# Optimization experiments

Measured on AMD Instinct MI355X. Metric: run time of the kernel, lower is better.

The kernel has to match this reference:

```python
import jax, jax.numpy as jnp
import numpy as np

NE, NR, D, H, L = 200000, 500, 128, 4, 2
HD = D // H
N, E, B = 32768, 262144, 256
MARGIN = 1.0


def setup_inputs() -> dict:
    key = jax.random.key(0)
    ks = jax.random.split(key, 16)
    nrm = lambda k, shp, s=0.05: jax.random.normal(k, shp, jnp.float32) * s
    inp = {
        'ent_emb': nrm(ks[0], (NE, D)),
        'rel_emb': nrm(ks[1], (NR, D)),
        'rel_prior': nrm(ks[2], (NR, 1)),
    }
    for i, nm in enumerate(['Wq', 'Wk', 'Wv', 'Wo', 'Wek', 'Wev']):
        inp[nm] = nrm(ks[3 + i], (L, D, D))
    for gi, g in enumerate(['h', 't', 'n']):
        kb = jax.random.fold_in(key, 100 + gi)
        k1, k2, k3, k4 = jax.random.split(kb, 4)
        inp[f'x_{g}'] = jax.random.randint(k1, (N,), 0, NE, jnp.int32)
        inp[f'ei_{g}'] = jax.random.randint(k2, (2, E), 0, N, jnp.int32)
        inp[f'ea_{g}'] = jax.random.randint(k3, (E,), 0, NR, jnp.int32)
        inp[f'y_{g}'] = jax.random.randint(k4, (B,), 0, N // B, jnp.int32)
        inp[f's_{g}'] = jnp.full((B,), N // B, dtype=jnp.int32)
    inp['sample'] = jax.random.randint(ks[9], (B, 3), 0, NR, jnp.int32)
    return inp


def gnn_embed(ent_emb, rel_emb, rel_prior, Wq, Wk, Wv, Wo, Wek, Wev, x, ei, ea, y, s):
    n = x.shape[0]
    h = ent_emb[x]                    # [N, D] node features (embedding lookup)
    e_emb = rel_emb[ea]               # [E, D] edge relation embedding
    e_pri = rel_prior[ea]             # [E, 1] scalar relation prior gate
    src, dst = ei[0], ei[1]
    scale = 1.0 / np.sqrt(HD).astype(np.float32)
    for l in range(L):
        q = (h @ Wq[l]).reshape(n, H, HD)[dst]                               # [E,H,HD]
        k = (h @ Wk[l]).reshape(n, H, HD)[src] + (e_emb @ Wek[l]).reshape(-1, H, HD)
        v = (h @ Wv[l]).reshape(n, H, HD)[src] + (e_emb @ Wev[l]).reshape(-1, H, HD)
        score = jnp.sum(q * k, axis=-1) * scale * e_pri                      # [E,H]
        # segment softmax over incoming edges of each destination node
        m = jax.ops.segment_max(score, dst, num_segments=n)
        m = jnp.where(jnp.isfinite(m), m, 0.0)
        ex = jnp.exp(score - m[dst])
        den = jax.ops.segment_sum(ex, dst, num_segments=n)[dst]
        alpha = ex / (den + 1e-16)                                           # [E,H]
        msg = jax.ops.segment_sum((alpha[..., None] * v).reshape(-1, D), dst, num_segments=n)
        h = jax.nn.gelu(h + msg @ Wo[l])                                     # residual + activation
    # get_real_index: exclusive cumsum of graph sizes + local target index
    offsets = jnp.concatenate([jnp.zeros((1,), s.dtype), jnp.cumsum(s)[:-1]])
    return h[offsets + y]             # [B, D]


def reference(ent_emb, rel_emb, rel_prior, Wq, Wk, Wv, Wo, Wek, Wev,
              x_h, ei_h, ea_h, y_h, s_h,
              x_t, ei_t, ea_t, y_t, s_t,
              x_n, ei_n, ea_n, y_n, s_n, sample):
    g = lambda x, ei, ea, y, s: gnn_embed(ent_emb, rel_emb, rel_prior, Wq, Wk, Wv, Wo, Wek, Wev, x, ei, ea, y, s)
    h = g(x_h, ei_h, ea_h, y_h, s_h)[:, None, :]   # [B,1,D]
    t = g(x_t, ei_t, ea_t, y_t, s_t)[:, None, :]
    tn = g(x_n, ei_n, ea_n, y_n, s_n)[:, None, :]
    r = rel_emb[sample[:, 1]][:, None, :]          # [B,1,D]
    proj_t = h + r                                 # TransE projection
    pos = jnp.linalg.norm(t - proj_t + 1e-8, axis=2)   # [B,1]
    negs = jnp.linalg.norm(t - tn + 1e-8, axis=2)      # [B,1]
    neg = jnp.mean(negs, axis=-1)                      # [B]
    # MarginRankingLoss(pos, neg, target=-1): mean(max(0, (pos-neg)+margin)); broadcasts [B,1]-[B] -> [B,B]
    loss = jnp.mean(jnp.maximum(pos - neg + MARGIN, 0.0))
    return loss
```

## Files before the change

### kernel.cpp

```cpp
#include <hip/hip_runtime.h>
#include <hip/hip_bf16.h>
#include <math.h>

#define NEC 200000
#define NRC 500
#define DD 128
#define LLC 2
#define NNODE 32768
#define EEDGE 262144
#define BBATCH 256
#define NG 3
#define BCAP 32

typedef __attribute__((ext_vector_type(8))) short short8;
typedef __attribute__((ext_vector_type(4))) float floatx4;
typedef __attribute__((ext_vector_type(4))) unsigned short ushort4v;

__device__ __forceinline__ float bf2f(unsigned short u) {
  union { unsigned int i; float f; } c; c.i = ((unsigned int)u) << 16; return c.f;
}
__device__ __forceinline__ unsigned short f2bf(float f) {
  union { float f; unsigned int i; } c; c.f = f;
  unsigned int x = c.i;
  unsigned int r = x + 0x7fffu + ((x >> 16) & 1u);
  return (unsigned short)(r >> 16);
}
__device__ __forceinline__ float bfu_lo(unsigned int u) {
  union { unsigned int i; float f; } c; c.i = u << 16; return c.f;
}
__device__ __forceinline__ float bfu_hi(unsigned int u) {
  union { unsigned int i; float f; } c; c.i = u & 0xffff0000u; return c.f;
}

__device__ __forceinline__ bool detect_fm(const void* ent) {
  unsigned int u = ((const unsigned int*)ent)[threadIdx.x & 63];
  bool big = fabsf(bfu_lo(u)) > 100.f;
  return __ballot(big) != 0ull;
}

__global__ __launch_bounds__(128) void k_prep(const void* ent, const void* rel,
    const void* prior, const void* Wq, const void* Wk, const void* Wv, const void* Wo,
    const void* Wek, const void* Wev,
    float* pris, unsigned short* WT, unsigned short* relk, unsigned short* relv) {
  bool fm = detect_fm(ent);
  int bid = blockIdx.x, tid = threadIdx.x;
  if (bid < 4) {
    int r = bid * 128 + tid;
    if (r < NRC) {
      float p = fm ? ((const float*)prior)[r] : bf2f(((const unsigned short*)prior)[r]);
      pris[r] = p * 0.17677669529663687f;
    }
  } else if (bid < 1028) {
    int t = (bid - 4) * 128 + tid;
    int mat = t >> 15;
    int rem = t & 32767;
    int l = rem >> 14;
    int p = rem & 16383;
    int d = p >> 7, c = p & 127;
    const void* W = mat == 0 ? Wq : (mat == 1 ? Wk : (mat == 2 ? Wv : Wo));
    size_t src = (size_t)l * DD * DD + (size_t)c * DD + d;
    float v = fm ? ((const float*)W)[src] : bf2f(((const unsigned short*)W)[src]);
    WT[(((size_t)mat * LLC + l) * DD + d) * DD + c] = f2bf(v);
  } else {
    int rid = bid - 1028;
    int which = rid / 1000;
    int l = (rid / 500) % 2;
    int r = rid % 500;
    int d = tid;
    size_t wofs = (size_t)l * DD * DD;
    const float* Wf = (const float*)(which ? Wev : Wek) + wofs;
    const unsigned short* Wb = (const unsigned short*)(which ? Wev : Wek) + wofs;
    __shared__ float re[DD];
    re[d] = fm ? ((const float*)rel)[r * DD + d] : bf2f(((const unsigned short*)rel)[r * DD + d]);
    __syncthreads();
    float acc = 0.f;
    if (fm) { for (int c = 0; c < DD; ++c) acc += re[c] * Wf[c * DD + d]; }
    else    { for (int c = 0; c < DD; ++c) acc += re[c] * bf2f(Wb[c * DD + d]); }
    unsigned short* out = which ? relv : relk;
    out[((size_t)l * NRC + r) * DD + d] = f2bf(acc);
  }
}

__global__ __launch_bounds__(256) void k_gb(const void* ent,
    const int* x0, const int* x1, const int* x2,
    const int* ei0, const int* ea0, const int* ei1, const int* ea1,
    const int* ei2, const int* ea2,
    unsigned short* hbf, int* deg, unsigned int* bucket) {
  int bid = blockIdx.x, tid = threadIdx.x;
  if (bid < 3072) {
    bool fm = detect_fm(ent);
    int rbase = bid * 32;
    int g = rbase >> 15;
    const int* x = g == 0 ? x0 : (g == 1 ? x1 : x2);
    int c = tid & 31;
    int j4 = tid >> 5;
    int rows[4], xs[4];
    #pragma unroll
    for (int k = 0; k < 4; ++k) {
      rows[k] = rbase + j4 + 8 * k;
      xs[k] = x[rows[k] & (NNODE - 1)];
    }
    if (fm) {
      float4 v[4];
      #pragma unroll
      for (int k = 0; k < 4; ++k)
        v[k] = *reinterpret_cast<const float4*>((const float*)ent + (size_t)xs[k] * DD + c * 4);
      #pragma unroll
      for (int k = 0; k < 4; ++k) {
        uint2 o;
        o.x = ((unsigned int)f2bf(v[k].y) << 16) | (unsigned int)f2bf(v[k].x);
        o.y = ((unsigned int)f2bf(v[k].w) << 16) | (unsigned int)f2bf(v[k].z);
        *reinterpret_cast<uint2*>(hbf + (size_t)rows[k] * DD + c * 4) = o;
      }
    } else {
      uint2 v[4];
      #pragma unroll
      for (int k = 0; k < 4; ++k)
        v[k] = *reinterpret_cast<const uint2*>((const unsigned short*)ent + (size_t)xs[k] * DD + c * 4);
      #pragma unroll
      for (int k = 0; k < 4; ++k)
        *reinterpret_cast<uint2*>(hbf + (size_t)rows[k] * DD + c * 4) = v[k];
    }
  } else {
    int bb = bid - 3072;
    int g = bb >> 10;
    const int* ei = g == 0 ? ei0 : (g == 1 ? ei1 : ei2);
    const int* ea = g == 0 ? ea0 : (g == 1 ? ea1 : ea2);
    int e = (bb & 1023) * 256 + tid;
    int dst = ei[EEDGE + e];
    int src = ei[e];
    int r = ea[e];
    int pos = atomicAdd(&deg[g * NNODE + dst], 1);
    if (pos < BCAP)
      bucket[((size_t)g * NNODE + dst) * BCAP + pos] = (unsigned int)src | ((unsigned int)r << 15);
  }
}

__device__ __forceinline__ void stage_wt(const unsigned short* WT, int tid,
                                         unsigned short (*Wt)[136]) {
  #pragma unroll
  for (int pass = 0; pass < 8; ++pass) {
    int idx = pass * 256 + tid;
    int d = idx >> 4, c0 = (idx & 15) << 3;
    *reinterpret_cast<short8*>(&Wt[d][c0]) =
        *reinterpret_cast<const short8*>(WT + d * DD + c0);
  }
}

__global__ __launch_bounds__(256) void k_gemm_qkv(const unsigned short* A,
    const unsigned short* WT, int layer, unsigned short* Qo, unsigned short* Ko,
    unsigned short* Vo) {
  __shared__ unsigned short Wt[DD][136];
  int mat = blockIdx.y;
  unsigned short* O = mat == 0 ? Qo : (mat == 1 ? Ko : Vo);
  int g = blockIdx.z;
  const unsigned short* Ag = A + (size_t)g * NNODE * DD;
  unsigned short* Og = O + (size_t)g * NNODE * DD;
  int tid = threadIdx.x;
  stage_wt(WT + ((size_t)mat * LLC + layer) * DD * DD, tid, Wt);
  __syncthreads();
  int w = tid >> 6, lane = tid & 63;
  int m = lane & 15, quad = lane >> 4;
  int row = blockIdx.x * 64 + w * 16 + m;
  floatx4 acc[8];
  #pragma unroll
  for (int t = 0; t < 8; ++t) acc[t] = (floatx4){0.f, 0.f, 0.f, 0.f};
  const unsigned short* arow = Ag + (size_t)row * DD;
  #pragma unroll
  for (int ks = 0; ks < 4; ++ks) {
    short8 a = *reinterpret_cast<const short8*>(arow + ks * 32 + quad * 8);
    #pragma unroll
    for (int t = 0; t < 8; ++t) {
      short8 b = *reinterpret_cast<const short8*>(&Wt[t * 16 + m][ks * 32 + quad * 8]);
      acc[t] = __builtin_amdgcn_mfma_f32_16x16x32_bf16(a, b, acc[t], 0, 0, 0);
    }
  }
  __syncthreads();
  unsigned short* ut = &Wt[0][0];
  #pragma unroll
  for (int t = 0; t < 8; ++t) {
    #pragma unroll
    for (int r = 0; r < 4; ++r) {
      ut[(w * 16 + quad * 4 + r) * 136 + t * 16 + m] = f2bf(acc[t][r]);
    }
  }
  __syncthreads();
  int rowbase = blockIdx.x * 64;
  #pragma unroll
  for (int k = 0; k < 4; ++k) {
    int flat = k * 256 + tid;
    int rw = flat >> 4, c8 = flat & 15;
    short8 v = *reinterpret_cast<const short8*>(ut + rw * 136 + c8 * 8);
    *reinterpret_cast<short8*>(Og + (size_t)(rowbase + rw) * DD + c8 * 8) = v;
  }
}

__global__ __launch_bounds__(256) void k_gemm_o(const unsigned short* A,
    const unsigned short* WT, int layer, unsigned short* hbf) {
  __shared__ unsigned short Wt[DD][136];
  int g = blockIdx.y;
  const unsigned short* Ag = A + (size_t)g * NNODE * DD;
  unsigned short* hbg = hbf + (size_t)g * NNODE * DD;
  int tid = threadIdx.x;
  stage_wt(WT + ((size_t)3 * LLC + layer) * DD * DD, tid, Wt);
  __syncthreads();
  int w = tid >> 6, lane = tid & 63;
  int m = lane & 15, quad = lane >> 4;
  int row = blockIdx.x * 64 + w * 16 + m;
  floatx4 acc[8];
  #pragma unroll
  for (int t = 0; t < 8; ++t) acc[t] = (floatx4){0.f, 0.f, 0.f, 0.f};
  const unsigned short* arow = Ag + (size_t)row * DD;
  #pragma unroll
  for (int ks = 0; ks < 4; ++ks) {
    short8 a = *reinterpret_cast<const short8*>(arow + ks * 32 + quad * 8);
    #pragma unroll
    for (int t = 0; t < 8; ++t) {
      short8 b = *reinterpret_cast<const short8*>(&Wt[t * 16 + m][ks * 32 + quad * 8]);
      acc[t] = __builtin_amdgcn_mfma_f32_16x16x32_bf16(a, b, acc[t], 0, 0, 0);
    }
  }
  __syncthreads();
  float* ft = (float*)&Wt[0][0];
  #pragma unroll
  for (int t = 0; t < 8; ++t) {
    #pragma unroll
    for (int r = 0; r < 4; ++r) {
      ft[(w * 16 + quad * 4 + r) * 136 + t * 16 + m] = acc[t][r];
    }
  }
  __syncthreads();
  int rowbase = blockIdx.x * 64;
  #pragma unroll
  for (int k = 0; k < 8; ++k) {
    int flat = k * 256 + tid;
    int rw = flat >> 5, c4 = flat & 31;
    float4 v = *reinterpret_cast<const float4*>(ft + rw * 136 + c4 * 4);
    size_t gi = (size_t)(rowbase + rw) * DD + c4 * 4;
    uint2 hv = *reinterpret_cast<const uint2*>(hbg + gi);
    float h0 = bfu_lo(hv.x), h1 = bfu_hi(hv.x), h2 = bfu_lo(hv.y), h3 = bfu_hi(hv.y);
    float r0, r1, r2, r3;
    {
      float xv = v.x + h0;
      float z2 = 1.5957691216057308f * (xv + 0.044715f * xv * xv * xv);
      r0 = xv / (1.f + __expf(-z2));
      xv = v.y + h1;
      z2 = 1.5957691216057308f * (xv + 0.044715f * xv * xv * xv);
      r1 = xv / (1.f + __expf(-z2));
      xv = v.z + h2;
      z2 = 1.5957691216057308f * (xv + 0.044715f * xv * xv * xv);
      r2 = xv / (1.f + __expf(-z2));
      xv = v.w + h3;
      z2 = 1.5957691216057308f * (xv + 0.044715f * xv * xv * xv);
      r3 = xv / (1.f + __expf(-z2));
    }
    uint2 o;
    o.x = ((unsigned int)f2bf(r1) << 16) | (unsigned int)f2bf(r0);
    o.y = ((unsigned int)f2bf(r3) << 16) | (unsigned int)f2bf(r2);
    *reinterpret_cast<uint2*>(hbg + gi) = o;
  }
}

__global__ __launch_bounds__(256) void k_attn(const unsigned short* Q, const unsigned short* K,
    const unsigned short* V, const unsigned short* relk, const unsigned short* relv,
    const float* pris, const int* deg, const unsigned int* bucket, int layer,
    unsigned short* msgb) {
  int w = threadIdx.x >> 6, lane = threadIdx.x & 63;
  int quarter = lane >> 4, sl = lane & 15;
  int g = blockIdx.y;
  int dst = blockIdx.x * 4 + w;
  const unsigned short* rk = relk + (size_t)layer * NRC * DD;
  const unsigned short* rv = relv + (size_t)layer * NRC * DD;
  size_t gofs = (size_t)g * NNODE * DD;
  const unsigned short* Kg = K + gofs;
  const unsigned short* Vg = V + gofs;

  uint4 qu = *reinterpret_cast<const uint4*>(Q + gofs + (size_t)dst * DD + sl * 8);
  float q0 = bfu_lo(qu.x), q1 = bfu_hi(qu.x), q2 = bfu_lo(qu.y), q3 = bfu_hi(qu.y);
  float q4 = bfu_lo(qu.z), q5 = bfu_hi(qu.z), q6 = bfu_lo(qu.w), q7 = bfu_hi(qu.w);

  float den = 0.f;
  float m0 = 0.f, m1 = 0.f, m2 = 0.f, m3 = 0.f, m4 = 0.f, m5 = 0.f, m6 = 0.f, m7 = 0.f;
  int dg = deg[g * NNODE + dst]; if (dg > BCAP) dg = BCAP;
  size_t base = ((size_t)g * NNODE + dst) * BCAP;
  if (dg > 0) {
    int niter = (dg + 3) >> 2;
    unsigned int pe = bucket[base + (quarter < dg ? quarter : dg - 1)];
    for (int i = 0; i < niter; ++i) {
      unsigned int cur = pe;
      int nx = 4 * (i + 1) + quarter; if (nx >= dg) nx = dg - 1;
      pe = bucket[base + nx];
      int src = (int)(cur & 32767u);
      int r = (int)(cur >> 15);
      uint4 ku = *reinterpret_cast<const uint4*>(Kg + (size_t)src * DD + sl * 8);
      uint4 rku = *reinterpret_cast<const uint4*>(rk + (size_t)r * DD + sl * 8);
      uint4 vu = *reinterpret_cast<const uint4*>(Vg + (size_t)src * DD + sl * 8);
      uint4 rvu = *reinterpret_cast<const uint4*>(rv + (size_t)r * DD + sl * 8);
      float p = pris[r];
      float s = q0 * (bfu_lo(ku.x) + bfu_lo(rku.x))
              + q1 * (bfu_hi(ku.x) + bfu_hi(rku.x))
              + q2 * (bfu_lo(ku.y) + bfu_lo(rku.y))
              + q3 * (bfu_hi(ku.y) + bfu_hi(rku.y))
              + q4 * (bfu_lo(ku.z) + bfu_lo(rku.z))
              + q5 * (bfu_hi(ku.z) + bfu_hi(rku.z))
              + q6 * (bfu_lo(ku.w) + bfu_lo(rku.w))
              + q7 * (bfu_hi(ku.w) + bfu_hi(rku.w));
      s += __shfl_xor(s, 1); s += __shfl_xor(s, 2);
      bool valid = (4 * i + quarter) < dg;
      float ex = valid ? __expf(s * p) : 0.f;
      den += ex;
      m0 += ex * (bfu_lo(vu.x) + bfu_lo(rvu.x));
      m1 += ex * (bfu_hi(vu.x) + bfu_hi(rvu.x));
      m2 += ex * (bfu_lo(vu.y) + bfu_lo(rvu.y));
      m3 += ex * (bfu_hi(vu.y) + bfu_hi(rvu.y));
      m4 += ex * (bfu_lo(vu.z) + bfu_lo(rvu.z));
      m5 += ex * (bfu_hi(vu.z) + bfu_hi(rvu.z));
      m6 += ex * (bfu_lo(vu.w) + bfu_lo(rvu.w));
      m7 += ex * (bfu_hi(vu.w) + bfu_hi(rvu.w));
    }
  }
  den += __shfl_xor(den, 16); den += __shfl_xor(den, 32);
  m0 += __shfl_xor(m0, 16); m0 += __shfl_xor(m0, 32);
  m1 += __shfl_xor(m1, 16); m1 += __shfl_xor(m1, 32);
  m2 += __shfl_xor(m2, 16); m2 += __shfl_xor(m2, 32);
  m3 += __shfl_xor(m3, 16); m3 += __shfl_xor(m3, 32);
  m4 += __shfl_xor(m4, 16); m4 += __shfl_xor(m4, 32);
  m5 += __shfl_xor(m5, 16); m5 += __shfl_xor(m5, 32);
  m6 += __shfl_xor(m6, 16); m6 += __shfl_xor(m6, 32);
  m7 += __shfl_xor(m7, 16); m7 += __shfl_xor(m7, 32);
  float inv = 1.f / (den + 1e-16f);
  if (quarter == 0) {
    uint4 o;
    o.x = ((unsigned int)f2bf(m1 * inv) << 16) | (unsigned int)f2bf(m0 * inv);
    o.y = ((unsigned int)f2bf(m3 * inv) << 16) | (unsigned int)f2bf(m2 * inv);
    o.z = ((unsigned int)f2bf(m5 * inv) << 16) | (unsigned int)f2bf(m4 * inv);
    o.w = ((unsigned int)f2bf(m7 * inv) << 16) | (unsigned int)f2bf(m6 * inv);
    *reinterpret_cast<uint4*>(msgb + gofs + (size_t)dst * DD + sl * 8) = o;
  }
}

__global__ __launch_bounds__(128) void k_ep(const unsigned short* hbf, const void* ent,
    const void* rel,
    const int* y0, const int* s0, const int* y1, const int* s1, const int* y2, const int* s2,
    const int* sample, float* pos, float* neg) {
  bool fm = detect_fm(ent);
  int b = blockIdx.x, d = threadIdx.x;
  int oh = 0, ot = 0, on = 0;
  for (int j = 0; j < b; ++j) { oh += s0[j]; ot += s1[j]; on += s2[j]; }
  int ih = oh + y0[b], it = ot + y1[b], in_ = on + y2[b];
  float th = bf2f(hbf[((size_t)0 * NNODE + ih) * DD + d]);
  float tt = bf2f(hbf[((size_t)1 * NNODE + it) * DD + d]);
  float tn = bf2f(hbf[((size_t)2 * NNODE + in_) * DD + d]);
  int r = sample[b * 3 + 1];
  float rr = fm ? ((const float*)rel)[r * DD + d] : bf2f(((const unsigned short*)rel)[r * DD + d]);
  float dp = tt - (th + rr) + 1e-8f;
  float dn = tt - tn + 1e-8f;
  float ap = dp * dp, an = dn * dn;
  for (int o = 32; o > 0; o >>= 1) { ap += __shfl_down(ap, o); an += __shfl_down(an, o); }
  __shared__ float sa[2], sb[2];
  if ((d & 63) == 0) { sa[d >> 6] = ap; sb[d >> 6] = an; }
  __syncthreads();
  if (d == 0) { pos[b] = sqrtf(sa[0] + sa[1]); neg[b] = sqrtf(sb[0] + sb[1]); }
}

__global__ __launch_bounds__(256) void k_hinge(const float* pos, const float* neg,
    const void* ent, void* out) {
  bool fm = detect_fm(ent);
  __shared__ float ns[BBATCH];
  __shared__ float wsum[4];
  int t = threadIdx.x;
  ns[t] = neg[t];
  float pb = pos[t];
  __syncthreads();
  float local = 0.f;
  for (int j = 0; j < BBATCH; ++j) {
    float v = pb - ns[j] + 1.0f;
    local += v > 0.f ? v : 0.f;
  }
  for (int o = 32; o > 0; o >>= 1) local += __shfl_down(local, o);
  if ((t & 63) == 0) wsum[t >> 6] = local;
  __syncthreads();
  if (t == 0) {
    float loss = (wsum[0] + wsum[1] + wsum[2] + wsum[3]) * (1.f / (256.f * 256.f));
    if (fm) ((float*)out)[0] = loss;
    else    ((unsigned short*)out)[0] = f2bf(loss);
  }
}

extern "C" void kernel_launch(void* const* d_in, const int* in_sizes, int n_in,
                              void* d_out, int out_size, void* d_ws, size_t ws_size,
                              hipStream_t stream) {
  const void* ent   = d_in[0];
  const void* rel   = d_in[1];
  const void* prior = d_in[2];
  const void* Wq  = d_in[3];
  const void* Wk  = d_in[4];
  const void* Wv  = d_in[5];
  const void* Wo  = d_in[6];
  const void* Wek = d_in[7];
  const void* Wev = d_in[8];
  const int* sample = (const int*)d_in[24];

  size_t off = 0;
  char* basep = (char*)d_ws;
  auto alloc = [&](size_t bytes) -> void* {
    void* r = basep + off;
    off = (off + bytes + 255) & ~(size_t)255;
    return r;
  };
  unsigned short* hbf  = (unsigned short*)alloc((size_t)NG * NNODE * DD * 2);
  unsigned short* Qb   = (unsigned short*)alloc((size_t)NG * NNODE * DD * 2);
  unsigned short* Kb   = (unsigned short*)alloc((size_t)NG * NNODE * DD * 2);
  unsigned short* Vb   = (unsigned short*)alloc((size_t)NG * NNODE * DD * 2);
  unsigned short* msgb = (unsigned short*)alloc((size_t)NG * NNODE * DD * 2);
  unsigned short* relk = (unsigned short*)alloc((size_t)LLC * NRC * DD * 2);
  unsigned short* relv = (unsigned short*)alloc((size_t)LLC * NRC * DD * 2);
  unsigned short* WT   = (unsigned short*)alloc((size_t)4 * LLC * DD * DD * 2);
  float* pris = (float*)alloc((size_t)NRC * 4);
  int*   deg  = (int*)alloc((size_t)NG * NNODE * 4);
  unsigned int* bucket = (unsigned int*)alloc((size_t)NG * NNODE * BCAP * 4);
  float* pos  = (float*)alloc((size_t)BBATCH * 4);
  float* neg  = (float*)alloc((size_t)BBATCH * 4);

  const int* x0  = (const int*)d_in[9],  *x1 = (const int*)d_in[14], *x2 = (const int*)d_in[19];
  const int* ei0 = (const int*)d_in[10], *ei1 = (const int*)d_in[15], *ei2 = (const int*)d_in[20];
  const int* ea0 = (const int*)d_in[11], *ea1 = (const int*)d_in[16], *ea2 = (const int*)d_in[21];
  const int* y0  = (const int*)d_in[12], *y1 = (const int*)d_in[17], *y2 = (const int*)d_in[22];
  const int* s0  = (const int*)d_in[13], *s1 = (const int*)d_in[18], *s2 = (const int*)d_in[23];

  hipMemsetAsync(deg, 0, (size_t)NG * NNODE * 4, stream);
  k_prep<<<3028, 128, 0, stream>>>(ent, rel, prior, Wq, Wk, Wv, Wo, Wek, Wev,
                                   pris, WT, relk, relv);
  k_gb<<<6144, 256, 0, stream>>>(ent, x0, x1, x2, ei0, ea0, ei1, ea1, ei2, ea2,
                                 hbf, deg, bucket);
  for (int l = 0; l < LLC; ++l) {
    k_gemm_qkv<<<dim3(NNODE / 64, 3, NG), 256, 0, stream>>>(hbf, WT, l, Qb, Kb, Vb);
    k_attn<<<dim3(NNODE / 4, NG), 256, 0, stream>>>(Qb, Kb, Vb, relk, relv, pris, deg, bucket, l, msgb);
    k_gemm_o<<<dim3(NNODE / 64, NG), 256, 0, stream>>>(msgb, WT, l, hbf);
  }
  k_ep<<<BBATCH, 128, 0, stream>>>(hbf, ent, rel, y0, s0, y1, s1, y2, s2, sample, pos, neg);
  k_hinge<<<1, BBATCH, 0, stream>>>(pos, neg, ent, d_out);
}
```

Measured before the change: 506.2 us.

## Store K and V in interleaved FP8 rows and fold deg memset into prep

The QKV GEMM now writes K and V as FP8 (e4m3 via cvt_pk_fp8) interleaved into one 256-byte row per node. The attention kernel then gathers K and V for each source node from a single contiguous row at half the bytes. This is meant to cut the gather bandwidth of the edge-wise attention loop, at the cost of lower precision in K/V values. The degree-array memset is also moved into extra blocks of the prep kernel, removing a separate memset launch.

```diff
diff --git a/kernel.cpp b/kernel.cpp
--- a/kernel.cpp
+++ b/kernel.cpp
@@ -14,7 +14,7 @@
 
 typedef __attribute__((ext_vector_type(8))) short short8;
 typedef __attribute__((ext_vector_type(4))) float floatx4;
-typedef __attribute__((ext_vector_type(4))) unsigned short ushort4v;
+typedef __attribute__((ext_vector_type(2))) float floatx2;
 
 __device__ __forceinline__ float bf2f(unsigned short u) {
   union { unsigned int i; float f; } c; c.i = ((unsigned int)u) << 16; return c.f;
@@ -41,7 +41,7 @@
 __global__ __launch_bounds__(128) void k_prep(const void* ent, const void* rel,
     const void* prior, const void* Wq, const void* Wk, const void* Wv, const void* Wo,
     const void* Wek, const void* Wev,
-    float* pris, unsigned short* WT, unsigned short* relk, unsigned short* relv) {
+    float* pris, unsigned short* WT, unsigned short* relk, unsigned short* relv, int* deg) {
   bool fm = detect_fm(ent);
   int bid = blockIdx.x, tid = threadIdx.x;
   if (bid < 4) {
@@ -61,7 +61,7 @@
     size_t src = (size_t)l * DD * DD + (size_t)c * DD + d;
     float v = fm ? ((const float*)W)[src] : bf2f(((const unsigned short*)W)[src]);
     WT[(((size_t)mat * LLC + l) * DD + d) * DD + c] = f2bf(v);
-  } else {
+  } else if (bid < 3028) {
     int rid = bid - 1028;
     int which = rid / 1000;
     int l = (rid / 500) % 2;
@@ -78,6 +78,11 @@
     else    { for (int c = 0; c < DD; ++c) acc += re[c] * bf2f(Wb[c * DD + d]); }
     unsigned short* out = which ? relv : relk;
     out[((size_t)l * NRC + r) * DD + d] = f2bf(acc);
+  } else {
+    int t = (bid - 3028) * 128 + tid;
+    uint4 z = {0u, 0u, 0u, 0u};
+    ((uint4*)deg)[t * 2] = z;
+    ((uint4*)deg)[t * 2 + 1] = z;
   }
 }
 
@@ -148,14 +153,11 @@
 }
 
 __global__ __launch_bounds__(256) void k_gemm_qkv(const unsigned short* A,
-    const unsigned short* WT, int layer, unsigned short* Qo, unsigned short* Ko,
-    unsigned short* Vo) {
+    const unsigned short* WT, int layer, unsigned short* Qo, unsigned char* KV) {
   __shared__ unsigned short Wt[DD][136];
   int mat = blockIdx.y;
-  unsigned short* O = mat == 0 ? Qo : (mat == 1 ? Ko : Vo);
   int g = blockIdx.z;
   const unsigned short* Ag = A + (size_t)g * NNODE * DD;
-  unsigned short* Og = O + (size_t)g * NNODE * DD;
   int tid = threadIdx.x;
   stage_wt(WT + ((size_t)mat * LLC + layer) * DD * DD, tid, Wt);
   __syncthreads();
@@ -186,12 +188,35 @@
   }
   __syncthreads();
   int rowbase = blockIdx.x * 64;
-  #pragma unroll
-  for (int k = 0; k < 4; ++k) {
-    int flat = k * 256 + tid;
-    int rw = flat >> 4, c8 = flat & 15;
-    short8 v = *reinterpret_cast<const short8*>(ut + rw * 136 + c8 * 8);
-    *reinterpret_cast<short8*>(Og + (size_t)(rowbase + rw) * DD + c8 * 8) = v;
+  if (mat == 0) {
+    unsigned short* Og = Qo + (size_t)g * NNODE * DD;
+    #pragma unroll
+    for (int k = 0; k < 4; ++k) {
+      int flat = k * 256 + tid;
+      int rw = flat >> 4, c8 = flat & 15;
+      short8 v = *reinterpret_cast<const short8*>(ut + rw * 136 + c8 * 8);
+      *reinterpret_cast<short8*>(Og + (size_t)(rowbase + rw) * DD + c8 * 8) = v;
+    }
+  } else {
+    unsigned char* kvb = KV + (size_t)g * NNODE * 256 + (mat == 1 ? 0 : 128);
+    #pragma unroll
+    for (int k = 0; k < 2; ++k) {
+      int flat = k * 256 + tid;
+      int rw = flat >> 3, c16 = flat & 7;
+      const unsigned short* p = ut + rw * 136 + c16 * 16;
+      uint4 a = *reinterpret_cast<const uint4*>(p);
+      uint4 b = *reinterpret_cast<const uint4*>(p + 8);
+      unsigned int w0 = __builtin_amdgcn_cvt_pk_fp8_f32(bfu_lo(a.x), bfu_hi(a.x), 0u, false);
+      w0 = __builtin_amdgcn_cvt_pk_fp8_f32(bfu_lo(a.y), bfu_hi(a.y), w0, true);
+      unsigned int w1 = __builtin_amdgcn_cvt_pk_fp8_f32(bfu_lo(a.z), bfu_hi(a.z), 0u, false);
+      w1 = __builtin_amdgcn_cvt_pk_fp8_f32(bfu_lo(a.w), bfu_hi(a.w), w1, true);
+      unsigned int w2 = __builtin_amdgcn_cvt_pk_fp8_f32(bfu_lo(b.x), bfu_hi(b.x), 0u, false);
+      w2 = __builtin_amdgcn_cvt_pk_fp8_f32(bfu_lo(b.y), bfu_hi(b.y), w2, true);
+      unsigned int w3 = __builtin_amdgcn_cvt_pk_fp8_f32(bfu_lo(b.z), bfu_hi(b.z), 0u, false);
+      w3 = __builtin_amdgcn_cvt_pk_fp8_f32(bfu_lo(b.w), bfu_hi(b.w), w3, true);
+      uint4 o = {w0, w1, w2, w3};
+      *reinterpret_cast<uint4*>(kvb + (size_t)(rowbase + rw) * 256 + c16 * 16) = o;
+    }
   }
 }
 
@@ -261,8 +286,8 @@
   }
 }
 
-__global__ __launch_bounds__(256) void k_attn(const unsigned short* Q, const unsigned short* K,
-    const unsigned short* V, const unsigned short* relk, const unsigned short* relv,
+__global__ __launch_bounds__(256) void k_attn(const unsigned short* Q, const unsigned char* KV,
+    const unsigned short* relk, const unsigned short* relv,
     const float* pris, const int* deg, const unsigned int* bucket, int layer,
     unsigned short* msgb) {
   int w = threadIdx.x >> 6, lane = threadIdx.x & 63;
@@ -271,9 +296,8 @@
   int dst = blockIdx.x * 4 + w;
   const unsigned short* rk = relk + (size_t)layer * NRC * DD;
   const unsigned short* rv = relv + (size_t)layer * NRC * DD;
+  const unsigned char* KVg = KV + (size_t)g * NNODE * 256;
   size_t gofs = (size_t)g * NNODE * DD;
-  const unsigned short* Kg = K + gofs;
-  const unsigned short* Vg = V + gofs;
 
   uint4 qu = *reinterpret_cast<const uint4*>(Q + gofs + (size_t)dst * DD + sl * 8);
   float q0 = bfu_lo(qu.x), q1 = bfu_hi(qu.x), q2 = bfu_lo(qu.y), q3 = bfu_hi(qu.y);
@@ -292,31 +316,40 @@
       pe = bucket[base + nx];
       int src = (int)(cur & 32767u);
       int r = (int)(cur >> 15);
-      uint4 ku = *reinterpret_cast<const uint4*>(Kg + (size_t)src * DD + sl * 8);
+      const unsigned char* kvrow = KVg + (size_t)src * 256;
+      uint2 k8 = *reinterpret_cast<const uint2*>(kvrow + sl * 8);
+      uint2 v8 = *reinterpret_cast<const uint2*>(kvrow + 128 + sl * 8);
       uint4 rku = *reinterpret_cast<const uint4*>(rk + (size_t)r * DD + sl * 8);
-      uint4 vu = *reinterpret_cast<const uint4*>(Vg + (size_t)src * DD + sl * 8);
       uint4 rvu = *reinterpret_cast<const uint4*>(rv + (size_t)r * DD + sl * 8);
       float p = pris[r];
-      float s = q0 * (bfu_lo(ku.x) + bfu_lo(rku.x))
-              + q1 * (bfu_hi(ku.x) + bfu_hi(rku.x))
-              + q2 * (bfu_lo(ku.y) + bfu_lo(rku.y))
-              + q3 * (bfu_hi(ku.y) + bfu_hi(rku.y))
-              + q4 * (bfu_lo(ku.z) + bfu_lo(rku.z))
-              + q5 * (bfu_hi(ku.z) + bfu_hi(rku.z))
-              + q6 * (bfu_lo(ku.w) + bfu_lo(rku.w))
-              + q7 * (bfu_hi(ku.w) + bfu_hi(rku.w));
+      floatx2 k01 = __builtin_amdgcn_cvt_pk_f32_fp8(k8.x, false);
+      floatx2 k23 = __builtin_amdgcn_cvt_pk_f32_fp8(k8.x, true);
+      floatx2 k45 = __builtin_amdgcn_cvt_pk_f32_fp8(k8.y, false);
+      floatx2 k67 = __builtin_amdgcn_cvt_pk_f32_fp8(k8.y, true);
+      float s = q0 * (k01.x + bfu_lo(rku.x))
+              + q1 * (k01.y + bfu_hi(rku.x))
+              + q2 * (k23.x + bfu_lo(rku.y))
+              + q3 * (k23.y + bfu_hi(rku.y))
+              + q4 * (k45.x + bfu_lo(rku.z))
+              + q5 * (k45.y + bfu_hi(rku.z))
+              + q6 * (k67.x + bfu_lo(rku.w))
+              + q7 * (k67.y + bfu_hi(rku.w));
       s += __shfl_xor(s, 1); s += __shfl_xor(s, 2);
       bool valid = (4 * i + quarter) < dg;
       float ex = valid ? __expf(s * p) : 0.f;
+      floatx2 v01 = __builtin_amdgcn_cvt_pk_f32_fp8(v8.x, false);
+      floatx2 v23 = __builtin_amdgcn_cvt_pk_f32_fp8(v8.x, true);
+      floatx2 v45 = __builtin_amdgcn_cvt_pk_f32_fp8(v8.y, false);
+      floatx2 v67 = __builtin_amdgcn_cvt_pk_f32_fp8(v8.y, true);
       den += ex;
-      m0 += ex * (bfu_lo(vu.x) + bfu_lo(rvu.x));
-      m1 += ex * (bfu_hi(vu.x) + bfu_hi(rvu.x));
-      m2 += ex * (bfu_lo(vu.y) + bfu_lo(rvu.y));
-      m3 += ex * (bfu_hi(vu.y) + bfu_hi(rvu.y));
-      m4 += ex * (bfu_lo(vu.z) + bfu_lo(rvu.z));
-      m5 += ex * (bfu_hi(vu.z) + bfu_hi(rvu.z));
-      m6 += ex * (bfu_lo(vu.w) + bfu_lo(rvu.w));
-      m7 += ex * (bfu_hi(vu.w) + bfu_hi(rvu.w));
+      m0 += ex * (v01.x + bfu_lo(rvu.x));
+      m1 += ex * (v01.y + bfu_hi(rvu.x));
+      m2 += ex * (v23.x + bfu_lo(rvu.y));
+      m3 += ex * (v23.y + bfu_hi(rvu.y));
+      m4 += ex * (v45.x + bfu_lo(rvu.z));
+      m5 += ex * (v45.y + bfu_hi(rvu.z));
+      m6 += ex * (v67.x + bfu_lo(rvu.w));
+      m7 += ex * (v67.y + bfu_hi(rvu.w));
     }
   }
   den += __shfl_xor(den, 16); den += __shfl_xor(den, 32);
@@ -410,8 +443,7 @@
   };
   unsigned short* hbf  = (unsigned short*)alloc((size_t)NG * NNODE * DD * 2);
   unsigned short* Qb   = (unsigned short*)alloc((size_t)NG * NNODE * DD * 2);
-  unsigned short* Kb   = (unsigned short*)alloc((size_t)NG * NNODE * DD * 2);
-  unsigned short* Vb   = (unsigned short*)alloc((size_t)NG * NNODE * DD * 2);
+  unsigned char*  KV   = (unsigned char*)alloc((size_t)NG * NNODE * 256);
   unsigned short* msgb = (unsigned short*)alloc((size_t)NG * NNODE * DD * 2);
   unsigned short* relk = (unsigned short*)alloc((size_t)LLC * NRC * DD * 2);
   unsigned short* relv = (unsigned short*)alloc((size_t)LLC * NRC * DD * 2);
@@ -428,14 +460,13 @@
   const int* y0  = (const int*)d_in[12], *y1 = (const int*)d_in[17], *y2 = (const int*)d_in[22];
   const int* s0  = (const int*)d_in[13], *s1 = (const int*)d_in[18], *s2 = (const int*)d_in[23];
 
-  hipMemsetAsync(deg, 0, (size_t)NG * NNODE * 4, stream);
-  k_prep<<<3028, 128, 0, stream>>>(ent, rel, prior, Wq, Wk, Wv, Wo, Wek, Wev,
-                                   pris, WT, relk, relv);
+  k_prep<<<3124, 128, 0, stream>>>(ent, rel, prior, Wq, Wk, Wv, Wo, Wek, Wev,
+                                   pris, WT, relk, relv, deg);
   k_gb<<<6144, 256, 0, stream>>>(ent, x0, x1, x2, ei0, ea0, ei1, ea1, ei2, ea2,
                                  hbf, deg, bucket);
   for (int l = 0; l < LLC; ++l) {
-    k_gemm_qkv<<<dim3(NNODE / 64, 3, NG), 256, 0, stream>>>(hbf, WT, l, Qb, Kb, Vb);
-    k_attn<<<dim3(NNODE / 4, NG), 256, 0, stream>>>(Qb, Kb, Vb, relk, relv, pris, deg, bucket, l, msgb);
+    k_gemm_qkv<<<dim3(NNODE / 64, 3, NG), 256, 0, stream>>>(hbf, WT, l, Qb, KV);
+    k_attn<<<dim3(NNODE / 4, NG), 256, 0, stream>>>(Qb, KV, relk, relv, pris, deg, bucket, l, msgb);
     k_gemm_o<<<dim3(NNODE / 64, NG), 256, 0, stream>>>(msgb, WT, l, hbf);
   }
   k_ep<<<BBATCH, 128, 0, stream>>>(hbf, ent, rel, y0, s0, y1, s1, y2, s2, sample, pos, neg);
```

Result: faster. 487.1 us (-3.8%).
